# Kernel optimization log

Measured on AMD Instinct MI355X. Metric: run time of the kernel, lower is better.

The kernel has to match this reference:

```python
import jax, jax.numpy as jnp
import numpy as np


def setup_inputs() -> dict:
    key = jax.random.key(0)
    k0, k1, k2, k3, k4, k5 = jax.random.split(key, 6)
    N, E, F, D, H = 50000, 1000000, 128, 32, 4
    # xavier_normal with gain = calculate_gain('relu') = sqrt(2)
    std = np.sqrt(2.0) * np.sqrt(2.0 / (F + D))
    return {
        "entity_features": jax.random.normal(k0, (N, 1, F), jnp.float32),
        "relation_features": jax.random.normal(k1, (E, 1, F), jnp.float32),
        "src": jax.random.randint(k2, (E,), 0, N, jnp.int32),
        "dst": jax.random.randint(k3, (E,), 0, N, jnp.int32),
        "w_q": jax.random.normal(k4, (H, F, D), jnp.float32) * std,
        "w_k": jax.random.normal(k5, (H, F, D), jnp.float32) * std,
    }


def reference(entity_features, relation_features, src, dst, w_q, w_k):
    # entity_features: (N, 1, F) -> repeat over heads is just a broadcast
    feat = entity_features[:, 0, :]        # (N, F)
    rel = relation_features[:, 0, :]       # (E, F)
    num_heads = w_q.shape[0]
    N = feat.shape[0]

    # per-head projections: q = feat @ w_q, k = feat @ w_k, erel = rel @ w_k
    q = jnp.einsum("nf,hfd->nhd", feat, w_q)      # (N, H, D)  'out_el'
    k = jnp.einsum("nf,hfd->nhd", feat, w_k)      # (N, H, D)  'out_er'
    erel = jnp.einsum("ef,hfd->ehd", rel, w_k)    # (E, H, D)  'out_erel'

    # v_dot_u: dst's out_er . src's out_el ; e_dot_u: edge out_erel . src's out_er
    e = (jnp.einsum("ehd,ehd->eh", k[dst], q[src])
         + jnp.einsum("ehd,ehd->eh", erel, k[src]))   # (E, H)
    e = jax.nn.leaky_relu(e, negative_slope=0.01)

    # edge_softmax normalized by source node (softmax over outgoing edges)
    m = jax.ops.segment_max(e, src, num_segments=N)   # (N, H)
    m = jnp.where(jnp.isfinite(m), m, jnp.zeros_like(m))
    ex = jnp.exp(e - m[src])                          # (E, H)
    denom = jax.ops.segment_sum(ex, src, num_segments=N)  # (N, H)
    att = ex / denom[src]                             # (E, H)

    # squeeze(-1).sum(-1)/num_heads on the (E, H, 1) edge tensor -> mean over heads
    return att.sum(axis=-1) / num_heads               # (E,)
```

## Files before the change

### kernel.cpp

```cpp
#include <hip/hip_runtime.h>

#define HH 4
#define FF 128
#define DD 32

typedef float f32x4 __attribute__((ext_vector_type(4)));


__global__ void zero_kernel(int* __restrict__ c, int n) {
    int i = blockIdx.x * blockDim.x + threadIdx.x;
    if (i < n) c[i] = 0;
}

__global__ __launch_bounds__(256) void scan_partial_kernel(int* __restrict__ partial, int nb) {
    __shared__ int sm[256];
    int t = threadIdx.x;
    int v = (t < nb) ? partial[t] : 0;
    sm[t] = v; __syncthreads();
    for (int off = 1; off < 256; off <<= 1) {
        int x = (t >= off) ? sm[t - off] : 0;
        __syncthreads();
        sm[t] += x;
        __syncthreads();
    }
    if (t < nb) partial[t] = sm[t] - v;
}

__global__ void addback_kernel(int* __restrict__ start, int* __restrict__ cursor,
                               const int* __restrict__ partial, int N) {
    int gid = blockIdx.x * 256 + threadIdx.x;
    if (gid < N) {
        int s = start[gid] + partial[blockIdx.x];
        start[gid] = s;
        cursor[gid] = s;
    }
}

__global__ void scatter_kernel(const int* __restrict__ src, const int* __restrict__ dst,
                               int* __restrict__ cursor, int* __restrict__ perm,
                               int* __restrict__ dsts, int E) {
    int i = blockIdx.x * blockDim.x + threadIdx.x;
    if (i >= E) return;
    int s = src[i];
    int pos = atomicAdd(&cursor[s], 1);
    perm[pos] = i;
    dsts[pos] = dst[i];
}


__global__ __launch_bounds__(256) void qk_hist_kernel(
    const float* __restrict__ feat, const float* __restrict__ wq,
    const float* __restrict__ wk, float* __restrict__ q,
    float* __restrict__ k, int N,
    const int* __restrict__ src, int* __restrict__ counts, int E, int QKB) {
    __shared__ float fs[32 * FF];
    int bid = blockIdx.x;
    if (bid >= QKB) {
        int i = ((bid - QKB) * 256 + threadIdx.x) * 4;
        if (i + 3 < E) {
            int4 v = *(const int4*)(src + i);
            atomicAdd(&counts[v.x], 1);
            atomicAdd(&counts[v.y], 1);
            atomicAdd(&counts[v.z], 1);
            atomicAdd(&counts[v.w], 1);
        } else {
            for (; i < E; ++i) atomicAdd(&counts[src[i]], 1);
        }
        return;
    }
    int n0 = bid * 32;
    int nb = N - n0; if (nb > 32) nb = 32;
    const float4* s4 = (const float4*)(feat + (size_t)n0 * FF);
    int nf4 = nb * FF / 4;
    for (int i = threadIdx.x; i < nf4; i += 256) ((float4*)fs)[i] = s4[i];
    __syncthreads();

    int isK = threadIdx.x >> 7;
    int o   = threadIdx.x & 127;
    int h = o >> 5, d = o & 31;
    const float* w = (isK ? wk : wq) + ((size_t)h * FF) * DD + d;

    float acc[32];
#pragma unroll
    for (int e = 0; e < 32; ++e) acc[e] = 0.f;
    for (int f = 0; f < FF; f += 4) {
        float w0 = w[(f + 0) * DD], w1 = w[(f + 1) * DD];
        float w2 = w[(f + 2) * DD], w3 = w[(f + 3) * DD];
#pragma unroll
        for (int e = 0; e < 32; ++e) {
            float4 fv = *(const float4*)&fs[e * FF + f];
            acc[e] += fv.x * w0 + fv.y * w1 + fv.z * w2 + fv.w * w3;
        }
    }
    float* outp = isK ? k : q;
    for (int e = 0; e < nb; ++e)
        outp[((size_t)(n0 + e) * HH + h) * DD + d] = acc[e];
}


__global__ __launch_bounds__(256) void kk_scan_kernel(
    const float* __restrict__ kbuf, const float* __restrict__ wk,
    float* __restrict__ kkout, int N,
    const int* __restrict__ counts, int* __restrict__ startb,
    int* __restrict__ partial, int KKB) {
    __shared__ float ks[16 * FF];
    __shared__ int sm[256];
    int bid = blockIdx.x;
    if (bid >= KKB) {
        int b = bid - KKB;
        int tid = threadIdx.x;
        int gid = b * 256 + tid;
        int v = gid < N ? counts[gid] : 0;
        sm[tid] = v; __syncthreads();
        for (int off = 1; off < 256; off <<= 1) {
            int x = (tid >= off) ? sm[tid - off] : 0;
            __syncthreads();
            sm[tid] += x;
            __syncthreads();
        }
        if (gid < N) startb[gid] = sm[tid] - v;
        if (tid == 255) partial[b] = sm[tid];
        return;
    }
    int n0 = bid * 16;
    int nb = N - n0; if (nb > 16) nb = 16;
    const float4* s4 = (const float4*)(kbuf + (size_t)n0 * FF);
    int nf4 = nb * FF / 4;
    for (int i = threadIdx.x; i < nf4; i += 256) ((float4*)ks)[i] = s4[i];
    __syncthreads();

    int o = threadIdx.x;
    int h1 = o >> 7, f1 = o & 127;
    int h2 = h1 + 2;
    const float* w1 = wk + ((size_t)h1 * FF + f1) * DD;
    const float* w2 = wk + ((size_t)h2 * FF + f1) * DD;

    float acc1[16], acc2[16];
#pragma unroll
    for (int e = 0; e < 16; ++e) { acc1[e] = 0.f; acc2[e] = 0.f; }
    for (int d = 0; d < DD; d += 4) {
        float4 wv1 = *(const float4*)&w1[d];
        float4 wv2 = *(const float4*)&w2[d];
#pragma unroll
        for (int e = 0; e < 16; ++e) {
            float4 k1 = *(const float4*)&ks[e * FF + h1 * DD + d];
            float4 k2 = *(const float4*)&ks[e * FF + h2 * DD + d];
            acc1[e] += k1.x * wv1.x + k1.y * wv1.y + k1.z * wv1.z + k1.w * wv1.w;
            acc2[e] += k2.x * wv2.x + k2.y * wv2.y + k2.z * wv2.z + k2.w * wv2.w;
        }
    }
    for (int e = 0; e < nb; ++e) {
        kkout[((size_t)(n0 + e) * HH + h1) * FF + f1] = acc1[e];
        kkout[((size_t)(n0 + e) * HH + h2) * FF + f1] = acc2[e];
    }
}


__device__ __forceinline__ int score4(
    const float* __restrict__ rel, const float* __restrict__ k,
    int pv, int dv, int j0, int g, int t,
    const float4* kkA, const float4* kkB, const float2* qv,
    float* ev, int* e_i_out) {
    int idx = j0 + g;
    int e_i = __shfl(pv, idx, 64);
    int dd  = __shfl(dv, idx, 64);
    *e_i_out = e_i;
    const float* rp = rel + (size_t)e_i * FF + t * 8;
    f32x4 r0 = __builtin_nontemporal_load((const f32x4*)rp);
    f32x4 r1 = __builtin_nontemporal_load((const f32x4*)(rp + 4));
#pragma unroll
    for (int h = 0; h < HH; ++h) {
        float2 kv = *(const float2*)(k + ((size_t)dd * HH + h) * DD + t * 2);
        float a = r0.x * kkA[h].x + r0.y * kkA[h].y + r0.z * kkA[h].z + r0.w * kkA[h].w
                + r1.x * kkB[h].x + r1.y * kkB[h].y + r1.z * kkB[h].z + r1.w * kkB[h].w
                + qv[h].x * kv.x + qv[h].y * kv.y;
#pragma unroll
        for (int off = 1; off < 16; off <<= 1) a += __shfl_xor(a, off, 64);
        ev[h] = a >= 0.f ? a : 0.01f * a;
    }
    return idx;
}

__global__ __launch_bounds__(256) void group_kernel(
    const float* __restrict__ rel, const int* __restrict__ perm,
    const int* __restrict__ dsts, const float* __restrict__ q,
    const float* __restrict__ k, const float* __restrict__ kk,
    const int* __restrict__ start, const int* __restrict__ counts,
    float* __restrict__ out, int N) {
    __shared__ __align__(16) float e_buf_all[4][128][4];
    int wid = threadIdx.x >> 6;
    int s = blockIdx.x * 4 + wid;
    if (s >= N) return;
    int cnt = counts[s];
    if (cnt == 0) return;
    int base = start[s];
    int lane = threadIdx.x & 63;
    int g = lane >> 4, t = lane & 15;
    float (*e_buf)[4] = e_buf_all[wid];

    float4 kkA[HH], kkB[HH];
    float2 qv[HH];
    const float* kkbase = kk + (size_t)s * (HH * FF) + t * 8;
    const float* qbase  = q  + (size_t)s * (HH * DD) + t * 2;
#pragma unroll
    for (int h = 0; h < HH; ++h) {
        kkA[h] = *(const float4*)(kkbase + h * FF);
        kkB[h] = *(const float4*)(kkbase + h * FF + 4);
        qv[h]  = *(const float2*)(qbase + h * DD);
    }

    float m[HH] = {-INFINITY, -INFINITY, -INFINITY, -INFINITY};
    bool fast = (cnt <= 128);

    for (int c0 = 0; c0 < cnt; c0 += 64) {
        int nc = min(cnt - c0, 64);
        int pv = 0, dv = 0;
        if (lane < nc) { pv = perm[base + c0 + lane]; dv = dsts[base + c0 + lane]; }
        for (int j0 = 0; j0 < nc; j0 += 4) {
            float ev[HH]; int e_i;
            int idx = score4(rel, k, pv, dv, j0, g, t, kkA, kkB, qv, ev, &e_i);
            if (idx < nc) {
#pragma unroll
                for (int h = 0; h < HH; ++h) m[h] = fmaxf(m[h], ev[h]);
                if (fast && t == 0)
                    *(float4*)e_buf[c0 + idx] = make_float4(ev[0], ev[1], ev[2], ev[3]);
            }
        }
    }
#pragma unroll
    for (int h = 0; h < HH; ++h) {
        m[h] = fmaxf(m[h], __shfl_xor(m[h], 16, 64));
        m[h] = fmaxf(m[h], __shfl_xor(m[h], 32, 64));
    }

    if (fast) {
        int i0 = lane, i1 = lane + 64;
        float ex0[HH] = {0.f, 0.f, 0.f, 0.f}, ex1[HH] = {0.f, 0.f, 0.f, 0.f};
        if (i0 < cnt) {
            float4 ev = *(const float4*)e_buf[i0];
            ex0[0] = __expf(ev.x - m[0]); ex0[1] = __expf(ev.y - m[1]);
            ex0[2] = __expf(ev.z - m[2]); ex0[3] = __expf(ev.w - m[3]);
        }
        if (i1 < cnt) {
            float4 ev = *(const float4*)e_buf[i1];
            ex1[0] = __expf(ev.x - m[0]); ex1[1] = __expf(ev.y - m[1]);
            ex1[2] = __expf(ev.z - m[2]); ex1[3] = __expf(ev.w - m[3]);
        }
        float rl[HH];
#pragma unroll
        for (int h = 0; h < HH; ++h) {
            float v = ex0[h] + ex1[h];
#pragma unroll
            for (int off = 1; off < 64; off <<= 1) v += __shfl_xor(v, off, 64);
            rl[h] = 1.0f / v;
        }
        if (i0 < cnt)
            out[perm[base + i0]] = 0.25f * (ex0[0]*rl[0] + ex0[1]*rl[1] + ex0[2]*rl[2] + ex0[3]*rl[3]);
        if (i1 < cnt)
            out[perm[base + i1]] = 0.25f * (ex1[0]*rl[0] + ex1[1]*rl[1] + ex1[2]*rl[2] + ex1[3]*rl[3]);
    } else {
        float lacc[HH] = {0.f, 0.f, 0.f, 0.f};
        for (int c0 = 0; c0 < cnt; c0 += 64) {
            int nc = min(cnt - c0, 64);
            int pv = 0, dv = 0;
            if (lane < nc) { pv = perm[base + c0 + lane]; dv = dsts[base + c0 + lane]; }
            for (int j0 = 0; j0 < nc; j0 += 4) {
                float ev[HH]; int e_i;
                int idx = score4(rel, k, pv, dv, j0, g, t, kkA, kkB, qv, ev, &e_i);
                if (idx < nc && t == 0) {
#pragma unroll
                    for (int h = 0; h < HH; ++h) lacc[h] += __expf(ev[h] - m[h]);
                }
            }
        }
        float rl[HH];
#pragma unroll
        for (int h = 0; h < HH; ++h) {
            float v = lacc[h];
#pragma unroll
            for (int off = 1; off < 64; off <<= 1) v += __shfl_xor(v, off, 64);
            rl[h] = 1.0f / v;
        }
        for (int c0 = 0; c0 < cnt; c0 += 64) {
            int nc = min(cnt - c0, 64);
            int pv = 0, dv = 0;
            if (lane < nc) { pv = perm[base + c0 + lane]; dv = dsts[base + c0 + lane]; }
            for (int j0 = 0; j0 < nc; j0 += 4) {
                float ev[HH]; int e_i;
                int idx = score4(rel, k, pv, dv, j0, g, t, kkA, kkB, qv, ev, &e_i);
                if (idx < nc && t == 0) {
                    float a = __expf(ev[0]-m[0])*rl[0] + __expf(ev[1]-m[1])*rl[1]
                            + __expf(ev[2]-m[2])*rl[2] + __expf(ev[3]-m[3])*rl[3];
                    out[e_i] = 0.25f * a;
                }
            }
        }
    }
}

extern "C" void kernel_launch(void* const* d_in, const int* in_sizes, int n_in,
                              void* d_out, int out_size, void* d_ws, size_t ws_size,
                              hipStream_t stream) {
    const float* feat = (const float*)d_in[0];
    const float* rel  = (const float*)d_in[1];
    const int*   src  = (const int*)d_in[2];
    const int*   dst  = (const int*)d_in[3];
    const float* wq   = (const float*)d_in[4];
    const float* wk   = (const float*)d_in[5];
    float* out = (float*)d_out;

    const int N = in_sizes[0] / FF;
    const int E = in_sizes[2];

    float* q      = (float*)d_ws;
    float* k      = q  + (size_t)N * HH * DD;
    float* kk     = k  + (size_t)N * HH * DD;
    int*   counts = (int*)(kk + (size_t)N * HH * FF);
    int*   start  = counts + N;
    int*   cursor = start + N;
    int*   partial= cursor + N;
    int*   perm   = partial + 256;
    int*   dsts   = perm + E;

    int nb  = (N + 255) / 256;
    int QKB = (N + 31) / 32;
    int HB  = (E + 1023) / 1024;
    int KKB = (N + 15) / 16;

    zero_kernel<<<nb, 256, 0, stream>>>(counts, N);
    qk_hist_kernel<<<QKB + HB, 256, 0, stream>>>(feat, wq, wk, q, k, N, src, counts, E, QKB);
    kk_scan_kernel<<<KKB + nb, 256, 0, stream>>>(k, wk, kk, N, counts, start, partial, KKB);
    scan_partial_kernel<<<1, 256, 0, stream>>>(partial, nb);
    addback_kernel<<<nb, 256, 0, stream>>>(start, cursor, partial, N);
    scatter_kernel<<<(E + 255) / 256, 256, 0, stream>>>(src, dst, cursor, perm, dsts, E);
    group_kernel<<<(N + 3) / 4, 256, 0, stream>>>(rel, perm, dsts, q, k, kk, start, counts, out, N);
}
```

Measured before the change: 416.3 us.

## Replace CSR scan with atomic wavefront allocation, prefetch edge loads, interleave k layout

The three-kernel exclusive scan is replaced by a wave-level shuffle scan plus an atomicAdd on a global cursor, which allocates non-sorted but contiguous segments per source node. The zero kernel becomes a memset. k is stored in an interleaved layout so each lane fetches its k values for all heads with two 16-byte loads. The group kernel's main loop software-prefetches the next edge's rel and k rows. Nontemporal loads and stores are added for kk, q and out. Together these cut launch count and hide gather latency, at the cost of more registers per thread and a segment order that is no longer deterministic.

Result: slower. 458.1 us (+10.0%).

```diff
diff --git a/kernel.cpp b/kernel.cpp
--- a/kernel.cpp
+++ b/kernel.cpp
@@ -5,36 +5,8 @@
 #define DD 32
 
 typedef float f32x4 __attribute__((ext_vector_type(4)));
-
-
-__global__ void zero_kernel(int* __restrict__ c, int n) {
-    int i = blockIdx.x * blockDim.x + threadIdx.x;
-    if (i < n) c[i] = 0;
-}
-
-__global__ __launch_bounds__(256) void scan_partial_kernel(int* __restrict__ partial, int nb) {
-    __shared__ int sm[256];
-    int t = threadIdx.x;
-    int v = (t < nb) ? partial[t] : 0;
-    sm[t] = v; __syncthreads();
-    for (int off = 1; off < 256; off <<= 1) {
-        int x = (t >= off) ? sm[t - off] : 0;
-        __syncthreads();
-        sm[t] += x;
-        __syncthreads();
-    }
-    if (t < nb) partial[t] = sm[t] - v;
-}
-
-__global__ void addback_kernel(int* __restrict__ start, int* __restrict__ cursor,
-                               const int* __restrict__ partial, int N) {
-    int gid = blockIdx.x * 256 + threadIdx.x;
-    if (gid < N) {
-        int s = start[gid] + partial[blockIdx.x];
-        start[gid] = s;
-        cursor[gid] = s;
-    }
-}
+typedef float f32x2 __attribute__((ext_vector_type(2)));
+
 
 __global__ void scatter_kernel(const int* __restrict__ src, const int* __restrict__ dst,
                                int* __restrict__ cursor, int* __restrict__ perm,
@@ -92,34 +64,43 @@
             acc[e] += fv.x * w0 + fv.y * w1 + fv.z * w2 + fv.w * w3;
         }
     }
-    float* outp = isK ? k : q;
-    for (int e = 0; e < nb; ++e)
-        outp[((size_t)(n0 + e) * HH + h) * DD + d] = acc[e];
-}
-
-
-__global__ __launch_bounds__(256) void kk_scan_kernel(
+    if (isK) {
+        int koff = (d >> 1) * 8 + h * 2 + (d & 1);
+        for (int e = 0; e < nb; ++e)
+            k[(size_t)(n0 + e) * FF + koff] = acc[e];
+    } else {
+        for (int e = 0; e < nb; ++e)
+            q[((size_t)(n0 + e) * HH + h) * DD + d] = acc[e];
+    }
+}
+
+
+__global__ __launch_bounds__(256) void kk_alloc_kernel(
     const float* __restrict__ kbuf, const float* __restrict__ wk,
     float* __restrict__ kkout, int N,
     const int* __restrict__ counts, int* __restrict__ startb,
-    int* __restrict__ partial, int KKB) {
+    int* __restrict__ cursor, int* __restrict__ gcur, int KKB) {
     __shared__ float ks[16 * FF];
-    __shared__ int sm[256];
     int bid = blockIdx.x;
     if (bid >= KKB) {
-        int b = bid - KKB;
-        int tid = threadIdx.x;
-        int gid = b * 256 + tid;
-        int v = gid < N ? counts[gid] : 0;
-        sm[tid] = v; __syncthreads();
-        for (int off = 1; off < 256; off <<= 1) {
-            int x = (tid >= off) ? sm[tid - off] : 0;
-            __syncthreads();
-            sm[tid] += x;
-            __syncthreads();
-        }
-        if (gid < N) startb[gid] = sm[tid] - v;
-        if (tid == 255) partial[b] = sm[tid];
+        int sid = (bid - KKB) * 256 + threadIdx.x;
+        int lane = threadIdx.x & 63;
+        int cnt = (sid < N) ? counts[sid] : 0;
+        int incl = cnt;
+#pragma unroll
+        for (int off = 1; off < 64; off <<= 1) {
+            int y = __shfl_up(incl, off, 64);
+            if (lane >= off) incl += y;
+        }
+        int total = __shfl(incl, 63, 64);
+        int base = 0;
+        if (lane == 63) base = atomicAdd(gcur, total);
+        base = __shfl(base, 63, 64);
+        if (sid < N) {
+            int st = base + incl - cnt;
+            startb[sid] = st;
+            cursor[sid] = st;
+        }
         return;
     }
     int n0 = bid * 16;
@@ -141,50 +122,52 @@
     for (int d = 0; d < DD; d += 4) {
         float4 wv1 = *(const float4*)&w1[d];
         float4 wv2 = *(const float4*)&w2[d];
+        int o0 = (d >> 1) * 8, o1 = o0 + 8;
 #pragma unroll
         for (int e = 0; e < 16; ++e) {
-            float4 k1 = *(const float4*)&ks[e * FF + h1 * DD + d];
-            float4 k2 = *(const float4*)&ks[e * FF + h2 * DD + d];
-            acc1[e] += k1.x * wv1.x + k1.y * wv1.y + k1.z * wv1.z + k1.w * wv1.w;
-            acc2[e] += k2.x * wv2.x + k2.y * wv2.y + k2.z * wv2.z + k2.w * wv2.w;
+            const float* kb = &ks[e * FF];
+            float2 a1 = *(const float2*)&kb[o0 + h1 * 2];
+            float2 b1 = *(const float2*)&kb[o1 + h1 * 2];
+            float2 a2 = *(const float2*)&kb[o0 + h2 * 2];
+            float2 b2 = *(const float2*)&kb[o1 + h2 * 2];
+            acc1[e] += a1.x * wv1.x + a1.y * wv1.y + b1.x * wv1.z + b1.y * wv1.w;
+            acc2[e] += a2.x * wv2.x + a2.y * wv2.y + b2.x * wv2.z + b2.y * wv2.w;
         }
     }
     for (int e = 0; e < nb; ++e) {
-        kkout[((size_t)(n0 + e) * HH + h1) * FF + f1] = acc1[e];
-        kkout[((size_t)(n0 + e) * HH + h2) * FF + f1] = acc2[e];
-    }
-}
-
-
-__device__ __forceinline__ int score4(
-    const float* __restrict__ rel, const float* __restrict__ k,
-    int pv, int dv, int j0, int g, int t,
-    const float4* kkA, const float4* kkB, const float2* qv,
-    float* ev, int* e_i_out) {
-    int idx = j0 + g;
-    int e_i = __shfl(pv, idx, 64);
-    int dd  = __shfl(dv, idx, 64);
-    *e_i_out = e_i;
+        __builtin_nontemporal_store(acc1[e], &kkout[((size_t)(n0 + e) * HH + h1) * FF + f1]);
+        __builtin_nontemporal_store(acc2[e], &kkout[((size_t)(n0 + e) * HH + h2) * FF + f1]);
+    }
+}
+
+
+__device__ __forceinline__ void score_one(
+    const float* __restrict__ rel, const float* __restrict__ k2,
+    int e_i, int dd, int t,
+    const float4* kkA, const float4* kkB, const float2* qv, float* ev) {
     const float* rp = rel + (size_t)e_i * FF + t * 8;
     f32x4 r0 = __builtin_nontemporal_load((const f32x4*)rp);
     f32x4 r1 = __builtin_nontemporal_load((const f32x4*)(rp + 4));
+    const float* kp = k2 + (size_t)dd * FF + t * 8;
+    f32x4 kva = *(const f32x4*)kp;
+    f32x4 kvb = *(const f32x4*)(kp + 4);
+    float kx[4] = {kva.x, kva.z, kvb.x, kvb.z};
+    float ky[4] = {kva.y, kva.w, kvb.y, kvb.w};
 #pragma unroll
     for (int h = 0; h < HH; ++h) {
-        float2 kv = *(const float2*)(k + ((size_t)dd * HH + h) * DD + t * 2);
         float a = r0.x * kkA[h].x + r0.y * kkA[h].y + r0.z * kkA[h].z + r0.w * kkA[h].w
                 + r1.x * kkB[h].x + r1.y * kkB[h].y + r1.z * kkB[h].z + r1.w * kkB[h].w
-                + qv[h].x * kv.x + qv[h].y * kv.y;
+                + qv[h].x * kx[h] + qv[h].y * ky[h];
 #pragma unroll
         for (int off = 1; off < 16; off <<= 1) a += __shfl_xor(a, off, 64);
         ev[h] = a >= 0.f ? a : 0.01f * a;
     }
-    return idx;
 }
 
 __global__ __launch_bounds__(256) void group_kernel(
     const float* __restrict__ rel, const int* __restrict__ perm,
     const int* __restrict__ dsts, const float* __restrict__ q,
-    const float* __restrict__ k, const float* __restrict__ kk,
+    const float* __restrict__ k2, const float* __restrict__ kk,
     const int* __restrict__ start, const int* __restrict__ counts,
     float* __restrict__ out, int N) {
     __shared__ __align__(16) float e_buf_all[4][128][4];
@@ -204,9 +187,12 @@
     const float* qbase  = q  + (size_t)s * (HH * DD) + t * 2;
 #pragma unroll
     for (int h = 0; h < HH; ++h) {
-        kkA[h] = *(const float4*)(kkbase + h * FF);
-        kkB[h] = *(const float4*)(kkbase + h * FF + 4);
-        qv[h]  = *(const float2*)(qbase + h * DD);
+        f32x4 a = __builtin_nontemporal_load((const f32x4*)(kkbase + h * FF));
+        f32x4 b = __builtin_nontemporal_load((const f32x4*)(kkbase + h * FF + 4));
+        kkA[h] = make_float4(a.x, a.y, a.z, a.w);
+        kkB[h] = make_float4(b.x, b.y, b.z, b.w);
+        f32x2 qb = __builtin_nontemporal_load((const f32x2*)(qbase + h * DD));
+        qv[h] = make_float2(qb.x, qb.y);
     }
 
     float m[HH] = {-INFINITY, -INFINITY, -INFINITY, -INFINITY};
@@ -216,15 +202,46 @@
         int nc = min(cnt - c0, 64);
         int pv = 0, dv = 0;
         if (lane < nc) { pv = perm[base + c0 + lane]; dv = dsts[base + c0 + lane]; }
+        int e0 = __shfl(pv, g, 64);
+        int d0 = __shfl(dv, g, 64);
+        const float* rp = rel + (size_t)e0 * FF + t * 8;
+        f32x4 r0 = __builtin_nontemporal_load((const f32x4*)rp);
+        f32x4 r1 = __builtin_nontemporal_load((const f32x4*)(rp + 4));
+        const float* kp = k2 + (size_t)d0 * FF + t * 8;
+        f32x4 kva = *(const f32x4*)kp;
+        f32x4 kvb = *(const f32x4*)(kp + 4);
+
         for (int j0 = 0; j0 < nc; j0 += 4) {
-            float ev[HH]; int e_i;
-            int idx = score4(rel, k, pv, dv, j0, g, t, kkA, kkB, qv, ev, &e_i);
-            if (idx < nc) {
+            int ni = (j0 + 4 + g) & 63;
+            int ne = __shfl(pv, ni, 64);
+            int nd = __shfl(dv, ni, 64);
+            const float* nrp = rel + (size_t)ne * FF + t * 8;
+            f32x4 nr0 = __builtin_nontemporal_load((const f32x4*)nrp);
+            f32x4 nr1 = __builtin_nontemporal_load((const f32x4*)(nrp + 4));
+            const float* nkp = k2 + (size_t)nd * FF + t * 8;
+            f32x4 nkva = *(const f32x4*)nkp;
+            f32x4 nkvb = *(const f32x4*)(nkp + 4);
+
+            float kx[4] = {kva.x, kva.z, kvb.x, kvb.z};
+            float ky[4] = {kva.y, kva.w, kvb.y, kvb.w};
+            float ev[HH];
+#pragma unroll
+            for (int h = 0; h < HH; ++h) {
+                float a = r0.x * kkA[h].x + r0.y * kkA[h].y + r0.z * kkA[h].z + r0.w * kkA[h].w
+                        + r1.x * kkB[h].x + r1.y * kkB[h].y + r1.z * kkB[h].z + r1.w * kkB[h].w
+                        + qv[h].x * kx[h] + qv[h].y * ky[h];
+#pragma unroll
+                for (int off = 1; off < 16; off <<= 1) a += __shfl_xor(a, off, 64);
+                ev[h] = a >= 0.f ? a : 0.01f * a;
+            }
+            int cidx = j0 + g;
+            if (cidx < nc) {
 #pragma unroll
                 for (int h = 0; h < HH; ++h) m[h] = fmaxf(m[h], ev[h]);
                 if (fast && t == 0)
-                    *(float4*)e_buf[c0 + idx] = make_float4(ev[0], ev[1], ev[2], ev[3]);
+                    *(float4*)e_buf[c0 + cidx] = make_float4(ev[0], ev[1], ev[2], ev[3]);
             }
+            r0 = nr0; r1 = nr1; kva = nkva; kvb = nkvb;
         }
     }
 #pragma unroll
@@ -255,9 +272,13 @@
             rl[h] = 1.0f / v;
         }
         if (i0 < cnt)
-            out[perm[base + i0]] = 0.25f * (ex0[0]*rl[0] + ex0[1]*rl[1] + ex0[2]*rl[2] + ex0[3]*rl[3]);
+            __builtin_nontemporal_store(
+                0.25f * (ex0[0]*rl[0] + ex0[1]*rl[1] + ex0[2]*rl[2] + ex0[3]*rl[3]),
+                &out[perm[base + i0]]);
         if (i1 < cnt)
-            out[perm[base + i1]] = 0.25f * (ex1[0]*rl[0] + ex1[1]*rl[1] + ex1[2]*rl[2] + ex1[3]*rl[3]);
+            __builtin_nontemporal_store(
+                0.25f * (ex1[0]*rl[0] + ex1[1]*rl[1] + ex1[2]*rl[2] + ex1[3]*rl[3]),
+                &out[perm[base + i1]]);
     } else {
         float lacc[HH] = {0.f, 0.f, 0.f, 0.f};
         for (int c0 = 0; c0 < cnt; c0 += 64) {
@@ -265,8 +286,11 @@
             int pv = 0, dv = 0;
             if (lane < nc) { pv = perm[base + c0 + lane]; dv = dsts[base + c0 + lane]; }
             for (int j0 = 0; j0 < nc; j0 += 4) {
-                float ev[HH]; int e_i;
-                int idx = score4(rel, k, pv, dv, j0, g, t, kkA, kkB, qv, ev, &e_i);
+                int idx = j0 + g;
+                int e_i = __shfl(pv, idx & 63, 64);
+                int dd  = __shfl(dv, idx & 63, 64);
+                float ev[HH];
+                score_one(rel, k2, e_i, dd, t, kkA, kkB, qv, ev);
                 if (idx < nc && t == 0) {
 #pragma unroll
                     for (int h = 0; h < HH; ++h) lacc[h] += __expf(ev[h] - m[h]);
@@ -286,8 +310,11 @@
             int pv = 0, dv = 0;
             if (lane < nc) { pv = perm[base + c0 + lane]; dv = dsts[base + c0 + lane]; }
             for (int j0 = 0; j0 < nc; j0 += 4) {
-                float ev[HH]; int e_i;
-                int idx = score4(rel, k, pv, dv, j0, g, t, kkA, kkB, qv, ev, &e_i);
+                int idx = j0 + g;
+                int e_i = __shfl(pv, idx & 63, 64);
+                int dd  = __shfl(dv, idx & 63, 64);
+                float ev[HH];
+                score_one(rel, k2, e_i, dd, t, kkA, kkB, qv, ev);
                 if (idx < nc && t == 0) {
                     float a = __expf(ev[0]-m[0])*rl[0] + __expf(ev[1]-m[1])*rl[1]
                             + __expf(ev[2]-m[2])*rl[2] + __expf(ev[3]-m[3])*rl[3];
@@ -313,13 +340,13 @@
     const int E = in_sizes[2];
 
     float* q      = (float*)d_ws;
-    float* k      = q  + (size_t)N * HH * DD;
-    float* kk     = k  + (size_t)N * HH * DD;
+    float* k2     = q  + (size_t)N * HH * DD;
+    float* kk     = k2 + (size_t)N * HH * DD;
     int*   counts = (int*)(kk + (size_t)N * HH * FF);
-    int*   start  = counts + N;
+    int*   gcur   = counts + N;
+    int*   start  = gcur + 1;
     int*   cursor = start + N;
-    int*   partial= cursor + N;
-    int*   perm   = partial + 256;
+    int*   perm   = cursor + N;
     int*   dsts   = perm + E;
 
     int nb  = (N + 255) / 256;
@@ -327,11 +354,9 @@
     int HB  = (E + 1023) / 1024;
     int KKB = (N + 15) / 16;
 
-    zero_kernel<<<nb, 256, 0, stream>>>(counts, N);
-    qk_hist_kernel<<<QKB + HB, 256, 0, stream>>>(feat, wq, wk, q, k, N, src, counts, E, QKB);
-    kk_scan_kernel<<<KKB + nb, 256, 0, stream>>>(k, wk, kk, N, counts, start, partial, KKB);
-    scan_partial_kernel<<<1, 256, 0, stream>>>(partial, nb);
-    addback_kernel<<<nb, 256, 0, stream>>>(start, cursor, partial, N);
+    hipMemsetAsync(counts, 0, (size_t)(N + 1) * sizeof(int), stream);
+    qk_hist_kernel<<<QKB + HB, 256, 0, stream>>>(feat, wq, wk, q, k2, N, src, counts, E, QKB);
+    kk_alloc_kernel<<<KKB + nb, 256, 0, stream>>>(k2, wk, kk, N, counts, start, cursor, gcur, KKB);
     scatter_kernel<<<(E + 255) / 256, 256, 0, stream>>>(src, dst, cursor, perm, dsts, E);
-    group_kernel<<<(N + 3) / 4, 256, 0, stream>>>(rel, perm, dsts, q, k, kk, start, counts, out, N);
-}
+    group_kernel<<<(N + 3) / 4, 256, 0, stream>>>(rel, perm, dsts, q, k2, kk, start, counts, out, N);
+}
```
